# Optimization experiments

Hardware: AMD Instinct MI355X
Metric: run time of the kernel (lower is better)

The kernel has to match this reference:

```python
import jax, jax.numpy as jnp
import numpy as np

N_NODES = 50000


def _gcn_conv(x, src, dst, W, b, n_nodes):
    # x: [N, Fin] -> h: [N, Fout]; GCN: D^-1/2 (A+I) D^-1/2 (x W) + b
    h = x @ W
    deg = jax.ops.segment_sum(jnp.ones_like(dst, dtype=h.dtype), dst,
                              num_segments=n_nodes)
    dinv = jax.lax.rsqrt(jnp.maximum(deg, 1.0))
    norm = dinv[src] * dinv[dst]                      # [E]
    msg = h[src] * norm[:, None]                      # [E, Fout] gather
    agg = jax.ops.segment_sum(msg, dst, num_segments=n_nodes)  # scatter-add
    return agg + b


def setup_inputs() -> dict:
    key = jax.random.key(0)
    k0, k1, k2, k3 = jax.random.split(key, 4)
    N, E, F_IN, H, C = N_NODES, 800000, 128, 128, 16
    x = jax.random.normal(k0, (N, F_IN), dtype=jnp.float32)
    edge_index = jax.random.randint(k1, (2, E), 0, N, dtype=jnp.int64)
    W1 = jax.random.normal(k2, (F_IN, H), dtype=jnp.float32) / np.sqrt(F_IN)
    b1 = jnp.zeros((H,), dtype=jnp.float32)
    W2 = jax.random.normal(k3, (H, C), dtype=jnp.float32) / np.sqrt(H)
    b2 = jnp.zeros((C,), dtype=jnp.float32)
    return {"x": x, "edge_index": edge_index, "W1": W1, "b1": b1,
            "W2": W2, "b2": b2}


def reference(x, edge_index, W1, b1, W2, b2):
    n = x.shape[0]
    # add self-loops (shared by both conv layers)
    loops = jnp.arange(n, dtype=edge_index.dtype)
    src = jnp.concatenate([edge_index[0], loops])
    dst = jnp.concatenate([edge_index[1], loops])
    h = _gcn_conv(x, src, dst, W1, b1, n)
    h = jax.nn.relu(h)
    # dropout p=0.5 is identity in eval mode
    h = _gcn_conv(h, src, dst, W2, b2, n)
    return jax.nn.log_softmax(h, axis=1)
```

## Files before the change

kernel.cpp:

```cpp
#include <hip/hip_runtime.h>
#include <hip/hip_fp16.h>
#include <math.h>


#define NBUCKET_SHIFT 8
#define BIN_CHUNK 4096
#define PAD_SLOP (15 << NBUCKET_SHIFT)
#define CAP  5120
#define CCAP (CAP + PAD_SLOP)

typedef __bf16 bf16x8 __attribute__((ext_vector_type(8)));
typedef float  f32x4  __attribute__((ext_vector_type(4)));
typedef float  f32x2  __attribute__((ext_vector_type(2)));

__device__ __forceinline__ unsigned short pack_bf16(float f) {
    unsigned u = __float_as_uint(f);
    return (unsigned short)((u + 0x7fffu + ((u >> 16) & 1u)) >> 16);
}

__device__ __forceinline__ void acc_fp8x16_fma(f32x2* a, uint4 v, float w) {
    f32x2 ww; ww.x = w; ww.y = w;
    a[0] += __builtin_amdgcn_cvt_pk_f32_fp8(v.x, false) * ww;
    a[1] += __builtin_amdgcn_cvt_pk_f32_fp8(v.x, true)  * ww;
    a[2] += __builtin_amdgcn_cvt_pk_f32_fp8(v.y, false) * ww;
    a[3] += __builtin_amdgcn_cvt_pk_f32_fp8(v.y, true)  * ww;
    a[4] += __builtin_amdgcn_cvt_pk_f32_fp8(v.z, false) * ww;
    a[5] += __builtin_amdgcn_cvt_pk_f32_fp8(v.z, true)  * ww;
    a[6] += __builtin_amdgcn_cvt_pk_f32_fp8(v.w, false) * ww;
    a[7] += __builtin_amdgcn_cvt_pk_f32_fp8(v.w, true)  * ww;
}

__device__ __forceinline__ void acc_fp16x8(f32x2* a, uint4 v) {
    float2 f;
    f = __half22float2(*(const __half2*)&v.x); a[0] += *(f32x2*)&f;
    f = __half22float2(*(const __half2*)&v.y); a[1] += *(f32x2*)&f;
    f = __half22float2(*(const __half2*)&v.z); a[2] += *(f32x2*)&f;
    f = __half22float2(*(const __half2*)&v.w); a[3] += *(f32x2*)&f;
}

union K1Smem {
    struct { unsigned spair[BIN_CHUNK]; int lcnt[256]; int lbase[256]; } b;
    unsigned short wtp[16384];
    float outb[4][16 * 132];
};

__global__ __launch_bounds__(256)
void bin_gemm1_kernel(const int* __restrict__ src, const int* __restrict__ dst,
                      int* __restrict__ bcur, unsigned* __restrict__ pairs,
                      int E, int nbuckets, int nbins,
                      const float* __restrict__ x, const float* __restrict__ W1,
                      unsigned* __restrict__ h1b, int N) {
    __shared__ K1Smem sm;
    const int blk = blockIdx.x;
    const int tid = threadIdx.x;

    if (blk < nbins) {
        const int e0 = blk * BIN_CHUNK;
        const int cnt = min(BIN_CHUNK, E - e0);
        sm.b.lcnt[tid] = 0;
        __syncthreads();
        for (int i = tid; i < cnt; i += 256) {
            unsigned s = (unsigned)src[e0 + i], d = (unsigned)dst[e0 + i];
            sm.b.spair[i] = (d >> NBUCKET_SHIFT) << 24 | (d & 255u) << 16 | s;
            atomicAdd(&sm.b.lcnt[d >> NBUCKET_SHIFT], 1);
        }
        __syncthreads();
        if (tid < nbuckets) {
            int c = sm.b.lcnt[tid];
            sm.b.lbase[tid] = (c > 0) ? atomicAdd(&bcur[tid], c) : 0;
            sm.b.lcnt[tid] = 0;
        }
        __syncthreads();
        for (int i = tid; i < cnt; i += 256) {
            unsigned p = sm.b.spair[i];
            int b = (int)(p >> 24);
            int off = atomicAdd(&sm.b.lcnt[b], 1);
            pairs[b * CAP + sm.b.lbase[b] + off] = p;
        }
        return;
    }

    const int gblk = blk - nbins;
    const int wave = tid >> 6, lane = tid & 63;
    const int q = lane >> 4, m = lane & 15;
    const int row0 = gblk * 64 + wave * 16;
    const int row = row0 + m;
    const int rowc = (row < N) ? row : (N - 1);

    for (int it = tid; it < 16384; it += 256) {
        int k = it >> 7, n = it & 127;
        int t = n >> 4, mm = n & 15;
        int ks = k >> 5;
        int lane2 = (((k & 31) >> 3) << 4) | mm;
        int j = k & 7;
        sm.wtp[(t * 4 + ks) * 512 + lane2 * 8 + j] = pack_bf16(W1[it]);
    }
    __syncthreads();

    f32x4 acc[8];
#pragma unroll
    for (int t = 0; t < 8; t++) acc[t] = (f32x4)0.0f;

#pragma unroll
    for (int ks = 0; ks < 4; ks++) {
        const float4* xp = (const float4*)(x + (size_t)rowc * 128 + ks * 32 + q * 8);
        float4 f0 = xp[0], f1 = xp[1];
        float fv[8] = {f0.x, f0.y, f0.z, f0.w, f1.x, f1.y, f1.z, f1.w};
        bf16x8 ah, al;
#pragma unroll
        for (int j = 0; j < 8; j++) {
            __bf16 h = (__bf16)fv[j];
            ah[j] = h;
            al[j] = (__bf16)(fv[j] - (float)h);
        }
#pragma unroll
        for (int t = 0; t < 8; t++) {
            bf16x8 b = *(const bf16x8*)(sm.wtp + (size_t)(t * 4 + ks) * 512 + lane * 8);
            acc[t] = __builtin_amdgcn_mfma_f32_16x16x32_bf16(ah, b, acc[t], 0, 0, 0);
            acc[t] = __builtin_amdgcn_mfma_f32_16x16x32_bf16(al, b, acc[t], 0, 0, 0);
        }
    }
    __syncthreads();

#pragma unroll
    for (int t = 0; t < 8; t++)
#pragma unroll
        for (int r = 0; r < 4; r++)
            sm.outb[wave][(q * 4 + r) * 132 + t * 16 + m] = acc[t][r];
    __syncthreads();

    const int r2 = lane >> 2, j = lane & 3;
    const int orow = row0 + r2;
    if (orow < N) {
        const float* lrow = &sm.outb[wave][r2 * 132];
#pragma unroll
        for (int s = 0; s < 4; s++) {
            float4 a = *(const float4*)(lrow + s * 32 + j * 8);
            float4 b = *(const float4*)(lrow + s * 32 + j * 8 + 4);
            unsigned lo = __builtin_amdgcn_cvt_pk_fp8_f32(a.x, a.y, 0, false);
            lo = __builtin_amdgcn_cvt_pk_fp8_f32(a.z, a.w, lo, true);
            unsigned hi = __builtin_amdgcn_cvt_pk_fp8_f32(b.x, b.y, 0, false);
            hi = __builtin_amdgcn_cvt_pk_fp8_f32(b.z, b.w, hi, true);
            ((uint2*)h1b)[(size_t)orow * 16 + s * 4 + j] = make_uint2(lo, hi);
        }
    }
}

__global__ __launch_bounds__(256)
void bucket_build_kernel(const int* __restrict__ bcur, const unsigned* __restrict__ pairs,
                         int* __restrict__ rowptr, int* __restrict__ rowcnt,
                         float* __restrict__ dinv, int* __restrict__ colsrc,
                         unsigned* __restrict__ h1b, unsigned* __restrict__ h2u,
                         int N, int nbuckets) {
    __shared__ int cnt[256];
    __shared__ int sm[256];
    const int tid = threadIdx.x;
    const int blk = blockIdx.x;
    const int nb0 = blk << NBUCKET_SHIFT;

    if (blk == 0) {
        if (tid < 32) h1b[(size_t)N * 32 + tid] = 0u;
        else if (tid < 40) h2u[(size_t)N * 8 + (tid - 32)] = 0u;
        else if (tid == 40) dinv[N] = 0.0f;
    }

    const int lo = blk * CAP;
    const int hi = lo + bcur[blk];
    cnt[tid] = 0;
    __syncthreads();

    for (int i = lo + tid; i < hi; i += 256)
        atomicAdd(&cnt[(int)(pairs[i] >> 16) & 255], 1);
    __syncthreads();

    int v = cnt[tid];
    int pdeg = (v + 15) & ~15;
    sm[tid] = pdeg;
    __syncthreads();
#pragma unroll
    for (int off = 1; off < 256; off <<= 1) {
        int u = (tid >= off) ? sm[tid - off] : 0;
        __syncthreads();
        sm[tid] += u;
        __syncthreads();
    }
    int pexcl = sm[tid] - pdeg;
    const int start = blk * CCAP + pexcl;
    int node = nb0 + tid;
    if (node < N) {
        rowptr[node] = start;
        rowcnt[node] = pdeg;
        dinv[node] = rsqrtf((float)v + 1.0f);
    }
    __syncthreads();
    cnt[tid] = start;
    __syncthreads();
    for (int i = lo + tid; i < hi; i += 256) {
        unsigned p = pairs[i];
        int pos = atomicAdd(&cnt[(int)(p >> 16) & 255], 1);
        colsrc[pos] = (int)(p & 0xffffu);
    }
    for (int p = start + v; p < start + pdeg; ++p)
        colsrc[p] = N;
}

__global__ __launch_bounds__(256)
void l1_fused_kernel(const int* __restrict__ rowptr, const int* __restrict__ rowcnt,
                     const int* __restrict__ colsrc,
                     const float* __restrict__ dinv, const unsigned* __restrict__ h1b,
                     const float* __restrict__ b1, const float* __restrict__ W2,
                     __half* __restrict__ h2s, int N) {
    __shared__ float rows[4][2][132];
    __shared__ float w2s[128 * 16];
    const int tid = threadIdx.x;
    const int wave = tid >> 6, lane = tid & 63;
    const int c = lane & 7;
    const int g = (lane >> 3) & 3;
    const int n = lane >> 5;
    const int d = blockIdx.x * 8 + wave * 2 + n;

    for (int i = tid; i < 512; i += 256)
        ((float4*)w2s)[i] = ((const float4*)W2)[i];

    const uint4* hq = (const uint4*)h1b;

    if (d < N) {
        const float dvd = dinv[d];
        f32x2 a[8];
#pragma unroll
        for (int j = 0; j < 8; j++) a[j] = (f32x2)0.0f;

        if (g == 0)
            acc_fp8x16_fma(a, hq[(size_t)d * 8 + c], dvd);

        int i = rowptr[d];
        const int end = i + rowcnt[d];
        int s0 = 0, s1 = 0, s2 = 0, s3 = 0;
        if (i < end) {
            s0 = colsrc[i + g];      s1 = colsrc[i + g + 4];
            s2 = colsrc[i + g + 8];  s3 = colsrc[i + g + 12];
        }
        while (i < end) {
            uint4 v0 = hq[(size_t)s0 * 8 + c];
            uint4 v1 = hq[(size_t)s1 * 8 + c];
            uint4 v2 = hq[(size_t)s2 * 8 + c];
            uint4 v3 = hq[(size_t)s3 * 8 + c];
            float w0 = dinv[s0], w1 = dinv[s1], w2 = dinv[s2], w3 = dinv[s3];
            i += 16;
            if (i < end) {
                s0 = colsrc[i + g];      s1 = colsrc[i + g + 4];
                s2 = colsrc[i + g + 8];  s3 = colsrc[i + g + 12];
            }
            acc_fp8x16_fma(a, v0, w0); acc_fp8x16_fma(a, v1, w1);
            acc_fp8x16_fma(a, v2, w2); acc_fp8x16_fma(a, v3, w3);
        }

#pragma unroll
        for (int j = 0; j < 8; j++) {
            a[j].x += __shfl_xor(a[j].x, 8, 64);
            a[j].y += __shfl_xor(a[j].y, 8, 64);
            a[j].x += __shfl_xor(a[j].x, 16, 64);
            a[j].y += __shfl_xor(a[j].y, 16, 64);
        }

        if (g == 0) {
            float* rbase = &rows[wave][n][c * 16];
#pragma unroll
            for (int t = 0; t < 4; t++) {
                float4 bb = ((const float4*)b1)[c * 4 + t];
                float4 o;
                o.x = fmaxf(a[2 * t].x * dvd + bb.x, 0.0f);
                o.y = fmaxf(a[2 * t].y * dvd + bb.y, 0.0f);
                o.z = fmaxf(a[2 * t + 1].x * dvd + bb.z, 0.0f);
                o.w = fmaxf(a[2 * t + 1].y * dvd + bb.w, 0.0f);
                *(float4*)(rbase + 4 * t) = o;
            }
        }
    }
    __syncthreads();

    const int n2 = lane >> 5, kh = (lane >> 4) & 1, col = lane & 15;
    const int d2 = blockIdx.x * 8 + wave * 2 + n2;
    if (d2 < N) {
        const float* r = &rows[wave][n2][kh * 64];
        const float* w = &w2s[kh * 64 * 16];
        float p = 0.0f;
#pragma unroll
        for (int k = 0; k < 64; k++)
            p = fmaf(r[k], w[k * 16 + col], p);
        p += __shfl_xor(p, 16, 64);
        if (kh == 0)
            h2s[(size_t)d2 * 16 + col] = __float2half_rn(p * dinv[d2]);
    }
}

__global__ __launch_bounds__(256)
void l2_kernel(const int* __restrict__ rowptr, const int* __restrict__ rowcnt,
               const int* __restrict__ colsrc,
               const float* __restrict__ dinv, const unsigned* __restrict__ h2s,
               const float* __restrict__ b2, float* __restrict__ out, int N) {
    const int tid = threadIdx.x;
    const int wave = tid >> 6, lane = tid & 63;
    const int n = lane >> 5;
    const int g = (lane >> 1) & 15;
    const int c = lane & 1;
    const int d = blockIdx.x * 8 + wave * 2 + n;
    if (d >= N) return;
    const uint4* h2q = (const uint4*)h2s;

    f32x2 a[4];
#pragma unroll
    for (int j = 0; j < 4; j++) a[j] = (f32x2)0.0f;

    if (g == 0)
        acc_fp16x8(a, h2q[(size_t)d * 2 + c]);

    int i = rowptr[d];
    const int end = i + rowcnt[d];
    int s = (i < end) ? colsrc[i + g] : 0;
    while (i < end) {
        uint4 v = h2q[(size_t)s * 2 + c];
        i += 16;
        if (i < end) s = colsrc[i + g];
        acc_fp16x8(a, v);
    }

#pragma unroll
    for (int j = 0; j < 4; j++) {
#pragma unroll
        for (int off = 2; off <= 16; off <<= 1) {
            a[j].x += __shfl_xor(a[j].x, off, 64);
            a[j].y += __shfl_xor(a[j].y, off, 64);
        }
    }

    const float dv = dinv[d];
    const float* af = (const float*)a;
    float v8[8];
#pragma unroll
    for (int j = 0; j < 8; j++) v8[j] = af[j] * dv + b2[c * 8 + j];

    float m = v8[0];
#pragma unroll
    for (int j = 1; j < 8; j++) m = fmaxf(m, v8[j]);
    m = fmaxf(m, __shfl_xor(m, 1, 64));
    float e = 0.0f;
#pragma unroll
    for (int j = 0; j < 8; j++) e += expf(v8[j] - m);
    e += __shfl_xor(e, 1, 64);
    float lse = m + logf(e);

    if (g == 0) {
        float4 o0 = make_float4(v8[0] - lse, v8[1] - lse, v8[2] - lse, v8[3] - lse);
        float4 o1 = make_float4(v8[4] - lse, v8[5] - lse, v8[6] - lse, v8[7] - lse);
        float4* op = (float4*)(out + (size_t)d * 16 + c * 8);
        op[0] = o0; op[1] = o1;
    }
}

extern "C" void kernel_launch(void* const* d_in, const int* in_sizes, int n_in,
                              void* d_out, int out_size, void* d_ws, size_t ws_size,
                              hipStream_t stream) {
    const float* x  = (const float*)d_in[0];
    const int*  ei  = (const int*)d_in[1];
    const float* W1 = (const float*)d_in[2];
    const float* b1 = (const float*)d_in[3];
    const float* W2 = (const float*)d_in[4];
    const float* b2 = (const float*)d_in[5];
    float* out = (float*)d_out;

    const int N = in_sizes[0] / 128;
    const int E = in_sizes[1] / 2;
    const int* src = ei;
    const int* dst = ei + E;
    const int nbuckets = (N + 255) >> NBUCKET_SHIFT;
    const int nbins = (E + BIN_CHUNK - 1) / BIN_CHUNK;
    const int g1blocks = (N + 63) / 64;

    float*          wsf     = (float*)d_ws;
    float*          dinv    = wsf;
    int*            rowptr  = (int*)(wsf + N + 16);
    int*            rowcnt  = rowptr + N;
    int*            bcur    = rowcnt + N;
    int*            colsrc  = bcur + 256;
    unsigned*       pairs   = (unsigned*)(colsrc + (size_t)nbuckets * CCAP);
    unsigned*       h1b     = pairs + (size_t)nbuckets * CAP;
    unsigned*       h2u     = h1b + (size_t)(N + 1) * 32;

    hipMemsetAsync(bcur, 0, 256 * sizeof(int), stream);
    bin_gemm1_kernel<<<nbins + g1blocks, 256, 0, stream>>>(src, dst, bcur, pairs,
                                                           E, nbuckets, nbins,
                                                           x, W1, h1b, N);

    bucket_build_kernel<<<nbuckets, 256, 0, stream>>>(bcur, pairs, rowptr, rowcnt,
                                                      dinv, colsrc, h1b, h2u,
                                                      N, nbuckets);

    l1_fused_kernel<<<(N + 7) / 8, 256, 0, stream>>>(rowptr, rowcnt, colsrc, dinv,
                                                     h1b, b1, W2, (__half*)h2u, N);

    l2_kernel<<<(N + 7) / 8, 256, 0, stream>>>(rowptr, rowcnt, colsrc, dinv, h2u,
                                               b2, out, N);
}
```

Measured before the change: 162.0 us.

## Cut CSR row padding to 8 and remap aggregation lanes per node

Row padding in the CSR build drops from multiples of 16 to multiples of 8. The layer-1 aggregation now gives each node a full wave (8 gather groups, 512-thread blocks) and prefetches the next gathered row one step ahead, instead of doing four outstanding loads per half-wave. Layer 2 packs four nodes per wave with 8 gather slots each. Less padding means fewer wasted gathers of the dummy zero row, especially for low-degree nodes. In exchange each lane has less memory-level parallelism per iteration, and there is an extra cross-lane reduction step.

```diff
diff --git a/kernel.cpp b/kernel.cpp
--- a/kernel.cpp
+++ b/kernel.cpp
@@ -5,7 +5,7 @@
 
 #define NBUCKET_SHIFT 8
 #define BIN_CHUNK 4096
-#define PAD_SLOP (15 << NBUCKET_SHIFT)
+#define PAD_SLOP (7 << NBUCKET_SHIFT)
 #define CAP  5120
 #define CCAP (CAP + PAD_SLOP)
 
@@ -174,7 +174,7 @@
     __syncthreads();
 
     int v = cnt[tid];
-    int pdeg = (v + 15) & ~15;
+    int pdeg = (v + 7) & ~7;
     sm[tid] = pdeg;
     __syncthreads();
 #pragma unroll
@@ -204,28 +204,28 @@
         colsrc[p] = N;
 }
 
-__global__ __launch_bounds__(256)
+__global__ __launch_bounds__(512, 8)
 void l1_fused_kernel(const int* __restrict__ rowptr, const int* __restrict__ rowcnt,
                      const int* __restrict__ colsrc,
                      const float* __restrict__ dinv, const unsigned* __restrict__ h1b,
                      const float* __restrict__ b1, const float* __restrict__ W2,
                      __half* __restrict__ h2s, int N) {
-    __shared__ float rows[4][2][132];
+    __shared__ float rows[8][132];
     __shared__ float w2s[128 * 16];
     const int tid = threadIdx.x;
     const int wave = tid >> 6, lane = tid & 63;
     const int c = lane & 7;
-    const int g = (lane >> 3) & 3;
-    const int n = lane >> 5;
-    const int d = blockIdx.x * 8 + wave * 2 + n;
-
-    for (int i = tid; i < 512; i += 256)
+    const int g = lane >> 3;
+    const int d = blockIdx.x * 8 + wave;
+
+    for (int i = tid; i < 512; i += 512)
         ((float4*)w2s)[i] = ((const float4*)W2)[i];
 
     const uint4* hq = (const uint4*)h1b;
+    float dvd = 0.0f;
 
     if (d < N) {
-        const float dvd = dinv[d];
+        dvd = dinv[d];
         f32x2 a[8];
 #pragma unroll
         for (int j = 0; j < 8; j++) a[j] = (f32x2)0.0f;
@@ -235,24 +235,22 @@
 
         int i = rowptr[d];
         const int end = i + rowcnt[d];
-        int s0 = 0, s1 = 0, s2 = 0, s3 = 0;
+        uint4 v; float w; int s2 = 0;
         if (i < end) {
-            s0 = colsrc[i + g];      s1 = colsrc[i + g + 4];
-            s2 = colsrc[i + g + 8];  s3 = colsrc[i + g + 12];
-        }
+            int s = colsrc[i + g];
+            v = hq[(size_t)s * 8 + c];
+            w = dinv[s];
+        }
+        if (i + 8 < end) s2 = colsrc[i + 8 + g];
         while (i < end) {
-            uint4 v0 = hq[(size_t)s0 * 8 + c];
-            uint4 v1 = hq[(size_t)s1 * 8 + c];
-            uint4 v2 = hq[(size_t)s2 * 8 + c];
-            uint4 v3 = hq[(size_t)s3 * 8 + c];
-            float w0 = dinv[s0], w1 = dinv[s1], w2 = dinv[s2], w3 = dinv[s3];
-            i += 16;
-            if (i < end) {
-                s0 = colsrc[i + g];      s1 = colsrc[i + g + 4];
-                s2 = colsrc[i + g + 8];  s3 = colsrc[i + g + 12];
+            uint4 vc = v; float wc = w;
+            if (i + 8 < end) {
+                v = hq[(size_t)s2 * 8 + c];
+                w = dinv[s2];
             }
-            acc_fp8x16_fma(a, v0, w0); acc_fp8x16_fma(a, v1, w1);
-            acc_fp8x16_fma(a, v2, w2); acc_fp8x16_fma(a, v3, w3);
+            if (i + 16 < end) s2 = colsrc[i + 16 + g];
+            i += 8;
+            acc_fp8x16_fma(a, vc, wc);
         }
 
 #pragma unroll
@@ -261,10 +259,12 @@
             a[j].y += __shfl_xor(a[j].y, 8, 64);
             a[j].x += __shfl_xor(a[j].x, 16, 64);
             a[j].y += __shfl_xor(a[j].y, 16, 64);
+            a[j].x += __shfl_xor(a[j].x, 32, 64);
+            a[j].y += __shfl_xor(a[j].y, 32, 64);
         }
 
         if (g == 0) {
-            float* rbase = &rows[wave][n][c * 16];
+            float* rbase = &rows[wave][c * 16];
 #pragma unroll
             for (int t = 0; t < 4; t++) {
                 float4 bb = ((const float4*)b1)[c * 4 + t];
@@ -279,18 +279,21 @@
     }
     __syncthreads();
 
-    const int n2 = lane >> 5, kh = (lane >> 4) & 1, col = lane & 15;
-    const int d2 = blockIdx.x * 8 + wave * 2 + n2;
-    if (d2 < N) {
-        const float* r = &rows[wave][n2][kh * 64];
-        const float* w = &w2s[kh * 64 * 16];
-        float p = 0.0f;
-#pragma unroll
-        for (int k = 0; k < 64; k++)
-            p = fmaf(r[k], w[k * 16 + col], p);
+    const int kq = lane >> 4, col = lane & 15;
+    if (d < N) {
+        const float* r = &rows[wave][kq * 32];
+        const float* w = &w2s[kq * 32 * 16];
+        float p0 = 0.0f, p1 = 0.0f;
+#pragma unroll
+        for (int k = 0; k < 16; k++) {
+            p0 = fmaf(r[k],      w[k * 16 + col],        p0);
+            p1 = fmaf(r[k + 16], w[(k + 16) * 16 + col], p1);
+        }
+        float p = p0 + p1;
         p += __shfl_xor(p, 16, 64);
-        if (kh == 0)
-            h2s[(size_t)d2 * 16 + col] = __float2half_rn(p * dinv[d2]);
+        p += __shfl_xor(p, 32, 64);
+        if (kq == 0)
+            h2s[(size_t)d * 16 + col] = __float2half_rn(p * dvd);
     }
 }
 
@@ -301,10 +304,10 @@
                const float* __restrict__ b2, float* __restrict__ out, int N) {
     const int tid = threadIdx.x;
     const int wave = tid >> 6, lane = tid & 63;
-    const int n = lane >> 5;
-    const int g = (lane >> 1) & 15;
+    const int n = lane >> 4;
+    const int g = (lane >> 1) & 7;
     const int c = lane & 1;
-    const int d = blockIdx.x * 8 + wave * 2 + n;
+    const int d = blockIdx.x * 16 + wave * 4 + n;
     if (d >= N) return;
     const uint4* h2q = (const uint4*)h2s;
 
@@ -317,18 +320,24 @@
 
     int i = rowptr[d];
     const int end = i + rowcnt[d];
-    int s = (i < end) ? colsrc[i + g] : 0;
+    uint4 v; int s2 = 0;
+    if (i < end) {
+        int s = colsrc[i + g];
+        v = h2q[(size_t)s * 2 + c];
+    }
+    if (i + 8 < end) s2 = colsrc[i + 8 + g];
     while (i < end) {
-        uint4 v = h2q[(size_t)s * 2 + c];
-        i += 16;
-        if (i < end) s = colsrc[i + g];
-        acc_fp16x8(a, v);
+        uint4 vc = v;
+        if (i + 8 < end) v = h2q[(size_t)s2 * 2 + c];
+        if (i + 16 < end) s2 = colsrc[i + 16 + g];
+        i += 8;
+        acc_fp16x8(a, vc);
     }
 
 #pragma unroll
     for (int j = 0; j < 4; j++) {
 #pragma unroll
-        for (int off = 2; off <= 16; off <<= 1) {
+        for (int off = 2; off <= 8; off <<= 1) {
             a[j].x += __shfl_xor(a[j].x, off, 64);
             a[j].y += __shfl_xor(a[j].y, off, 64);
         }
@@ -396,9 +405,9 @@
                                                       dinv, colsrc, h1b, h2u,
                                                       N, nbuckets);
 
-    l1_fused_kernel<<<(N + 7) / 8, 256, 0, stream>>>(rowptr, rowcnt, colsrc, dinv,
+    l1_fused_kernel<<<(N + 7) / 8, 512, 0, stream>>>(rowptr, rowcnt, colsrc, dinv,
                                                      h1b, b1, W2, (__half*)h2u, N);
 
-    l2_kernel<<<(N + 7) / 8, 256, 0, stream>>>(rowptr, rowcnt, colsrc, dinv, h2u,
-                                               b2, out, N);
-}
+    l2_kernel<<<(N + 15) / 16, 256, 0, stream>>>(rowptr, rowcnt, colsrc, dinv, h2u,
+                                                 b2, out, N);
+}
```

Result: slower. 174.7 us (+7.8%).
